# Performance work log

Measured on AMD Instinct MI355X. Metric: run time of the kernel, lower is better.

The kernel has to match this reference:

```python
import jax, jax.numpy as jnp
import numpy as np

N, D_IN, NUM, FRAME = 256, 3, 342, 100


def _make_w():
    # Faithful to the original: orthogonal factors U from SVD of random matrices,
    # seeded with 1234 (original uses np.random.seed(1234)).
    rng = np.random.RandomState(1234)
    w = np.zeros((D_IN, D_IN, NUM), dtype=np.float32)
    for i in range(NUM):
        a = rng.rand(D_IN, D_IN)
        u, _, _ = np.linalg.svd(a)
        w[:, :, i] = u.astype(np.float32)
    return jnp.asarray(w)


def setup_inputs() -> dict:
    key = jax.random.key(0)
    x = jax.random.normal(key, (N, D_IN, D_IN, NUM, FRAME), dtype=jnp.float32)
    w = _make_w()  # [D_in, D_in, num]
    return {"x": x, "w": w}


def reference(x, w):
    # Original: for each rotation index i, frame f, column slice along the second
    # D_in axis b, batch n:  Y[n, :, b, i, f] = w[:, :, i] @ x[n, :, b, i, f].
    # Collapse the triple Python loop into one batched contraction:
    #   Y[n,a,b,i,f] = sum_c w[a,c,i] * x[n,c,b,i,f]
    return jnp.einsum('aci,ncbif->nabif', w, x)
```

## Files before the change

### kernel.cpp

```cpp
#include <hip/hip_runtime.h>


typedef float f4 __attribute__((ext_vector_type(4)));

#define RN     256
#define RD     3
#define RNUM   342
#define RFRAME 100
#define RM     (RNUM * RFRAME)
#define RM4    (RM / 4)
#define RTOT4  (RN * RD * RM4)
#define RWSZ   (RD * RD * RNUM)
#define RCSTR4 (RD * RM / 4)

__device__ __forceinline__ void decomp(unsigned t, unsigned& base4, unsigned& i) {
    const unsigned m4 = t % RM4;
    const unsigned nb = t / RM4;
    i = m4 / 25;
    const unsigned n = nb / RD;
    const unsigned b = nb - n * RD;
    base4 = (n * (RD * RD) + b) * RM4 + m4;
}

__device__ __forceinline__ void compute_store(const float* __restrict__ wi,
                                              f4 x0, f4 x1, f4 x2,
                                              f4* __restrict__ yp) {
#pragma unroll
    for (int a = 0; a < RD; ++a) {
        const float wa0 = wi[(a * RD + 0) * RNUM];
        const float wa1 = wi[(a * RD + 1) * RNUM];
        const float wa2 = wi[(a * RD + 2) * RNUM];
        f4 o;
#pragma unroll
        for (int j = 0; j < 4; ++j)
            o[j] = fmaf(wa0, x0[j], fmaf(wa1, x1[j], wa2 * x2[j]));
        __builtin_nontemporal_store(o, yp + a * RCSTR4);
    }
}

__global__ __launch_bounds__(256) void
rotmap_kernel(const f4* __restrict__ x, const float* __restrict__ w,
              f4* __restrict__ y) {
    __shared__ float wlds[RWSZ];
    for (int idx = threadIdx.x; idx < RWSZ; idx += 256)
        wlds[idx] = w[idx];
    __syncthreads();

    const unsigned stride = gridDim.x * 256;
    unsigned t = blockIdx.x * 256 + threadIdx.x;

    while (t + stride < RTOT4) {
        unsigned baseA, iA, baseB, iB;
        decomp(t, baseA, iA);
        decomp(t + stride, baseB, iB);

        const f4* xa = x + baseA;
        const f4* xb = x + baseB;
        f4 a0 = __builtin_nontemporal_load(xa);
        f4 a1 = __builtin_nontemporal_load(xa + RCSTR4);
        f4 a2 = __builtin_nontemporal_load(xa + 2 * RCSTR4);
        f4 b0 = __builtin_nontemporal_load(xb);
        f4 b1 = __builtin_nontemporal_load(xb + RCSTR4);
        f4 b2 = __builtin_nontemporal_load(xb + 2 * RCSTR4);

        compute_store(&wlds[iA], a0, a1, a2, y + baseA);
        compute_store(&wlds[iB], b0, b1, b2, y + baseB);
        t += 2 * stride;
    }
    if (t < RTOT4) {
        unsigned base4, i;
        decomp(t, base4, i);
        const f4* xp = x + base4;
        f4 x0 = __builtin_nontemporal_load(xp);
        f4 x1 = __builtin_nontemporal_load(xp + RCSTR4);
        f4 x2 = __builtin_nontemporal_load(xp + 2 * RCSTR4);
        compute_store(&wlds[i], x0, x1, x2, y + base4);
    }
}

extern "C" void kernel_launch(void* const* d_in, const int* in_sizes, int n_in,
                              void* d_out, int out_size, void* d_ws, size_t ws_size,
                              hipStream_t stream) {
    const f4* x = (const f4*)d_in[0];
    const float* w = (const float*)d_in[1];
    f4* y = (f4*)d_out;

    rotmap_kernel<<<2048, 256, 0, stream>>>(x, w, y);
}
```

Baseline: 126.0 us.

## Transpose weights to per-row float4 in LDS, unroll loop by four, use plain loads

Rearranges the weight tensor in shared memory so each output row's three coefficients sit in one float4, turning three scalar LDS reads into one vector read. Doubles the per-iteration unroll from two to four grid-stride elements to keep more loads in flight, and adds a min-blocks occupancy hint to launch bounds. Input loads switch from nontemporal to ordinary cached loads, while stores stay nontemporal. The extra unroll raises register pressure, and the LDS setup now does index arithmetic per element.

```diff
diff --git a/kernel.cpp b/kernel.cpp
--- a/kernel.cpp
+++ b/kernel.cpp
@@ -10,8 +10,8 @@
 #define RM     (RNUM * RFRAME)
 #define RM4    (RM / 4)
 #define RTOT4  (RN * RD * RM4)
-#define RWSZ   (RD * RD * RNUM)
 #define RCSTR4 (RD * RM / 4)
+#define RWSRC  (RD * RD * RNUM)
 
 __device__ __forceinline__ void decomp(unsigned t, unsigned& base4, unsigned& i) {
     const unsigned m4 = t % RM4;
@@ -22,59 +22,63 @@
     base4 = (n * (RD * RD) + b) * RM4 + m4;
 }
 
-__device__ __forceinline__ void compute_store(const float* __restrict__ wi,
+__device__ __forceinline__ void compute_store(const f4* __restrict__ wt, unsigned i,
                                               f4 x0, f4 x1, f4 x2,
                                               f4* __restrict__ yp) {
+    const f4* wrow = wt + i * RD;
 #pragma unroll
     for (int a = 0; a < RD; ++a) {
-        const float wa0 = wi[(a * RD + 0) * RNUM];
-        const float wa1 = wi[(a * RD + 1) * RNUM];
-        const float wa2 = wi[(a * RD + 2) * RNUM];
+        const f4 wa = wrow[a];
         f4 o;
 #pragma unroll
         for (int j = 0; j < 4; ++j)
-            o[j] = fmaf(wa0, x0[j], fmaf(wa1, x1[j], wa2 * x2[j]));
+            o[j] = fmaf(wa.x, x0[j], fmaf(wa.y, x1[j], wa.z * x2[j]));
         __builtin_nontemporal_store(o, yp + a * RCSTR4);
     }
 }
 
-__global__ __launch_bounds__(256) void
+__global__ __launch_bounds__(256, 4) void
 rotmap_kernel(const f4* __restrict__ x, const float* __restrict__ w,
               f4* __restrict__ y) {
-    __shared__ float wlds[RWSZ];
-    for (int idx = threadIdx.x; idx < RWSZ; idx += 256)
-        wlds[idx] = w[idx];
+    __shared__ f4 wt[RNUM * RD];
+    for (int idx = threadIdx.x; idx < RWSRC; idx += 256) {
+        const int a = idx / (RD * RNUM);
+        const int rem = idx - a * RD * RNUM;
+        const int c = rem / RNUM;
+        const int i = rem - c * RNUM;
+        ((float*)&wt[i * RD + a])[c] = w[idx];
+    }
     __syncthreads();
 
     const unsigned stride = gridDim.x * 256;
     unsigned t = blockIdx.x * 256 + threadIdx.x;
 
-    while (t + stride < RTOT4) {
-        unsigned baseA, iA, baseB, iB;
-        decomp(t, baseA, iA);
-        decomp(t + stride, baseB, iB);
+    while (t + 3 * stride < RTOT4) {
+        unsigned bA, iA, bB, iB, bC, iC, bD, iD;
+        decomp(t,              bA, iA);
+        decomp(t + stride,     bB, iB);
+        decomp(t + 2 * stride, bC, iC);
+        decomp(t + 3 * stride, bD, iD);
 
-        const f4* xa = x + baseA;
-        const f4* xb = x + baseB;
-        f4 a0 = __builtin_nontemporal_load(xa);
-        f4 a1 = __builtin_nontemporal_load(xa + RCSTR4);
-        f4 a2 = __builtin_nontemporal_load(xa + 2 * RCSTR4);
-        f4 b0 = __builtin_nontemporal_load(xb);
-        f4 b1 = __builtin_nontemporal_load(xb + RCSTR4);
-        f4 b2 = __builtin_nontemporal_load(xb + 2 * RCSTR4);
+        const f4 *xa = x + bA, *xb = x + bB, *xc = x + bC, *xd = x + bD;
+        f4 a0 = xa[0], a1 = xa[RCSTR4], a2 = xa[2 * RCSTR4];
+        f4 b0 = xb[0], b1 = xb[RCSTR4], b2 = xb[2 * RCSTR4];
+        f4 c0 = xc[0], c1 = xc[RCSTR4], c2 = xc[2 * RCSTR4];
+        f4 d0 = xd[0], d1 = xd[RCSTR4], d2 = xd[2 * RCSTR4];
 
-        compute_store(&wlds[iA], a0, a1, a2, y + baseA);
-        compute_store(&wlds[iB], b0, b1, b2, y + baseB);
-        t += 2 * stride;
+        compute_store(wt, iA, a0, a1, a2, y + bA);
+        compute_store(wt, iB, b0, b1, b2, y + bB);
+        compute_store(wt, iC, c0, c1, c2, y + bC);
+        compute_store(wt, iD, d0, d1, d2, y + bD);
+        t += 4 * stride;
     }
-    if (t < RTOT4) {
-        unsigned base4, i;
-        decomp(t, base4, i);
-        const f4* xp = x + base4;
-        f4 x0 = __builtin_nontemporal_load(xp);
-        f4 x1 = __builtin_nontemporal_load(xp + RCSTR4);
-        f4 x2 = __builtin_nontemporal_load(xp + 2 * RCSTR4);
-        compute_store(&wlds[i], x0, x1, x2, y + base4);
+    while (t < RTOT4) {
+        unsigned b4, i;
+        decomp(t, b4, i);
+        const f4* xp = x + b4;
+        f4 x0 = xp[0], x1 = xp[RCSTR4], x2 = xp[2 * RCSTR4];
+        compute_store(wt, i, x0, x1, x2, y + b4);
+        t += stride;
     }
 }
 
```

Result: faster. 120.2 us (-4.7%).
